# Optimization experiments

Hardware: AMD Instinct MI355X
Metric: run time of the kernel (lower is better)

## Reference

```python
import jax, jax.numpy as jnp
import numpy as np

D_MODEL = 512
N_HEADS = 8
D_K = D_MODEL // N_HEADS


def setup_inputs() -> dict:
    key = jax.random.key(0)
    ks = jax.random.split(key, 9)
    s = 1.0 / np.sqrt(D_MODEL)
    x = jax.random.normal(ks[0], (2, 4096, D_MODEL), dtype=jnp.float32)
    def lin(kw, kb):
        W = jax.random.uniform(kw, (D_MODEL, D_MODEL), jnp.float32, -s, s)
        b = jax.random.uniform(kb, (D_MODEL,), jnp.float32, -s, s)
        return W, b
    Wq, bq = lin(ks[1], ks[2])
    Wk, bk = lin(ks[3], ks[4])
    Wv, bv = lin(ks[5], ks[6])
    Wo, bo = lin(ks[7], ks[8])
    return {"x": x, "Wq": Wq, "bq": bq, "Wk": Wk, "bk": bk,
            "Wv": Wv, "bv": bv, "Wo": Wo, "bo": bo}


def reference(x, Wq, bq, Wk, bk, Wv, bv, Wo, bo):
    B, T, C = x.shape
    # project and split heads: [B, H, T, d_k]
    def heads(W, b):
        return (x @ W.T + b).reshape(B, T, N_HEADS, D_K).transpose(0, 2, 1, 3)
    q = heads(Wq, bq)
    k = heads(Wk, bk)
    v = heads(Wv, bv)
    scores = jnp.einsum('bhqd,bhkd->bhqk', q, k) / np.sqrt(D_K).astype(jnp.float32)
    attn = jax.nn.softmax(scores, axis=-1)  # dropout p=0 (eval)
    out = jnp.einsum('bhqk,bhkd->bhqd', attn, v)
    out = out.transpose(0, 2, 1, 3).reshape(B, T, C)
    return out @ Wo.T + bo
```

## Files before the change

kernel.cpp:

```cpp
#include <hip/hip_runtime.h>

typedef _Float16 f16x8 __attribute__((ext_vector_type(8)));
typedef _Float16 f16x4 __attribute__((ext_vector_type(4)));
typedef _Float16 f16x2 __attribute__((ext_vector_type(2)));
typedef __fp16 hf16x2 __attribute__((ext_vector_type(2)));
typedef float f32x4 __attribute__((ext_vector_type(4)));

__device__ __forceinline__ float fast_exp2(float x) {
#if __has_builtin(__builtin_amdgcn_exp2f)
  return __builtin_amdgcn_exp2f(x);
#else
  return exp2f(x);
#endif
}

__device__ __forceinline__ f16x2 pk_cvt(float a, float b) {
#if __has_builtin(__builtin_amdgcn_cvt_pkrtz)
  union { hf16x2 h; f16x2 f; } u;
  u.h = __builtin_amdgcn_cvt_pkrtz(a, b);
  return u.f;
#else
  f16x2 r; r[0] = (_Float16)a; r[1] = (_Float16)b; return r;
#endif
}

__device__ __forceinline__ void qswap32(int& x, int& y) {
  asm("v_permlane32_swap_b32 %0, %1" : "+v"(x), "+v"(y));
}

__device__ __forceinline__ int swz23(int c) {
  return (c & ~12) | ((c & 4) << 1) | ((c & 8) >> 1);
}

__global__ void cvt_all(const float* __restrict__ x,
                        const float* __restrict__ Wq, const float* __restrict__ Wk,
                        const float* __restrict__ Wv, const float* __restrict__ Wo,
                        _Float16* __restrict__ xf, _Float16* __restrict__ wf) {
  int g = blockIdx.x * blockDim.x + threadIdx.x;
  const float* src;
  _Float16* dst;
  if (g < 524288) {
    src = x + (size_t)g * 8;
    dst = xf + (size_t)g * 8;
  } else {
    int g2 = g - 524288;
    int z = g2 >> 15, off = g2 & 32767;
    const float* W = (z == 0) ? Wq : (z == 1) ? Wk : (z == 2) ? Wv : Wo;
    src = W + (size_t)off * 8;
    dst = wf + (size_t)z * 262144 + (size_t)off * 8;
  }
  f32x4 a = *(const f32x4*)src;
  f32x4 b = *(const f32x4*)(src + 4);
  f16x8 o;
  o[0] = (_Float16)a[0]; o[1] = (_Float16)a[1];
  o[2] = (_Float16)a[2]; o[3] = (_Float16)a[3];
  o[4] = (_Float16)b[0]; o[5] = (_Float16)b[1];
  o[6] = (_Float16)b[2]; o[7] = (_Float16)b[3];
  *(f16x8*)dst = o;
}

__global__ __launch_bounds__(256, 2)
void qkv_gemm(const _Float16* __restrict__ X, const _Float16* __restrict__ Wf,
              const float* __restrict__ bq, const float* __restrict__ bk,
              const float* __restrict__ bv, _Float16* __restrict__ dst3) {
  __shared__ __align__(16) _Float16 As[128][72];
  __shared__ __align__(16) _Float16 Bs[128][72];
  const int z = blockIdx.z;
  const _Float16* Wz = Wf + (size_t)z * 262144;
  const float* bias = (z == 0) ? bq : (z == 1 ? bk : bv);
  _Float16* dst = dst3 + (size_t)z * 4194304;
  const float scale = (z == 0) ? 0.18033688011112042f : 1.0f;

  const int t = threadIdx.x;
  const int lane = t & 63, wave = t >> 6;
  const int quad = lane >> 4, col = lane & 15;
  const int wm = (wave & 1) * 64, wn = (wave >> 1) * 64;
  const int m0 = blockIdx.x * 128, n0 = blockIdx.y * 128;

  f32x4 acc[4][4] = {};

  for (int k0 = 0; k0 < 512; k0 += 64) {
    __syncthreads();
#pragma unroll
    for (int i = 0; i < 4; i++) {
      int flat = i * 2048 + t * 8;
      int r = flat >> 6, c = flat & 63;
      *(f16x8*)&As[r][c] = *(const f16x8*)&X[(size_t)(m0 + r) * 512 + k0 + c];
      *(f16x8*)&Bs[r][c] = *(const f16x8*)&Wz[(size_t)(n0 + r) * 512 + k0 + c];
    }
    __syncthreads();
#pragma unroll
    for (int ks = 0; ks < 2; ks++) {
      f16x8 a[4], b[4];
#pragma unroll
      for (int i = 0; i < 4; i++) {
        a[i] = *(const f16x8*)&As[wm + i * 16 + col][ks * 32 + quad * 8];
        b[i] = *(const f16x8*)&Bs[wn + i * 16 + col][ks * 32 + quad * 8];
      }
      if (z != 2) {
#pragma unroll
        for (int mi = 0; mi < 4; mi++)
#pragma unroll
          for (int ni = 0; ni < 4; ni++)
            acc[mi][ni] = __builtin_amdgcn_mfma_f32_16x16x32_f16(b[ni], a[mi], acc[mi][ni], 0, 0, 0);
      } else {
#pragma unroll
        for (int mi = 0; mi < 4; mi++)
#pragma unroll
          for (int ni = 0; ni < 4; ni++)
            acc[mi][ni] = __builtin_amdgcn_mfma_f32_16x16x32_f16(a[mi], b[ni], acc[mi][ni], 0, 0, 0);
      }
    }
  }

  if (z != 2) {
#pragma unroll
    for (int ni = 0; ni < 4; ni++) {
      int nb = n0 + wn + ni * 16 + quad * 4;
      int h = nb >> 6, d0 = nb & 63;
      f32x4 bb = *(const f32x4*)&bias[nb];
#pragma unroll
      for (int mi = 0; mi < 4; mi++) {
        int m = m0 + wm + mi * 16 + col;
        int b = m >> 12, tt = m & 4095;
        f16x4 ov;
#pragma unroll
        for (int r = 0; r < 4; r++)
          ov[r] = (_Float16)((acc[mi][ni][r] + bb[r]) * scale);
        *(f16x4*)&dst[((size_t)(b * 8 + h) * 4096 + tt) * 64 + d0] = ov;
      }
    }
  } else {
#pragma unroll
    for (int ni = 0; ni < 4; ni++) {
      int n = n0 + wn + ni * 16 + col;
      float bv_ = bias[n];
      int h = n >> 6, d = n & 63;
#pragma unroll
      for (int mi = 0; mi < 4; mi++) {
        int m = m0 + wm + mi * 16 + quad * 4;
        int b = m >> 12, tt = m & 4095;
        f16x4 ov;
#pragma unroll
        for (int r = 0; r < 4; r++) ov[r] = (_Float16)(acc[mi][ni][r] + bv_);
        *(f16x4*)&dst[((size_t)((b * 8 + h) * 64 + d)) * 4096 + tt] = ov;
      }
    }
  }
}

__global__ __launch_bounds__(256, 2)
void attn_kernel(const _Float16* __restrict__ Q, const _Float16* __restrict__ K,
                 const _Float16* __restrict__ V, _Float16* __restrict__ O) {
  __shared__ __align__(16) _Float16 Ks[2][128][72];
  __shared__ __align__(16) _Float16 Vt[2][64][136];

  const int t = threadIdx.x;
  const int lane = t & 63, wave = t >> 6;
  const int quad = lane >> 4, col = lane & 15;
  const int id = blockIdx.y * 32 + blockIdx.x;
  const int xcd = id & 7, slot = id >> 3;
  const int bh = xcd * 2 + (slot >> 5);
  const int q0 = (slot & 31) * 128;
  const _Float16* Qb = Q + (size_t)bh * 4096 * 64;
  const _Float16* Kbh = K + (size_t)bh * 4096 * 64;
  const _Float16* Vg = V + (size_t)bh * 64 * 4096;

  const int sr = (t * 8) >> 6, sc = (t * 8) & 63;
  const int vrow = t >> 4, vcol = (t & 15) * 8;
  const int vc0 = swz23(vcol);
  const int vc1 = swz23(vcol + 4);

  f16x8 qf[2][2];
#pragma unroll
  for (int mt = 0; mt < 2; mt++)
#pragma unroll
    for (int ks = 0; ks < 2; ks++)
      qf[mt][ks] = *(const f16x8*)&Qb[(size_t)(q0 + wave * 32 + mt * 16 + col) * 64 +
                                      ks * 32 + quad * 8];

  const f32x4 fz = {0.f, 0.f, 0.f, 0.f};

  f16x8 kreg[4], vreg[4];
#pragma unroll
  for (int i = 0; i < 4; i++)
    kreg[i] = *(const f16x8*)&Kbh[(size_t)(sr + 32 * i) * 64 + sc];
#pragma unroll
  for (int it = 0; it < 4; it++)
    vreg[it] = *(const f16x8*)&Vg[(size_t)(it * 16 + vrow) * 4096 + vcol];
#pragma unroll
  for (int i = 0; i < 4; i++)
    *(f16x8*)&Ks[0][sr + 32 * i][sc] = kreg[i];
#pragma unroll
  for (int it = 0; it < 4; it++) {
    f16x4 lo, hi;
#pragma unroll
    for (int u = 0; u < 4; u++) { lo[u] = vreg[it][u]; hi[u] = vreg[it][u + 4]; }
    *(f16x4*)&Vt[0][it * 16 + vrow][vc0] = lo;
    *(f16x4*)&Vt[0][it * 16 + vrow][vc1] = hi;
  }
  __syncthreads();

  f32x4 o_acc[2][4] = {};
  float lsum[2] = {0.f, 0.f};

  for (int j = 0; j < 32; j++) {
    const int buf = j & 1;
    if (j + 1 < 32) {
      const _Float16* Kb = Kbh + (size_t)(j + 1) * 128 * 64;
#pragma unroll
      for (int i = 0; i < 4; i++)
        kreg[i] = *(const f16x8*)&Kb[(size_t)(sr + 32 * i) * 64 + sc];
#pragma unroll
      for (int it = 0; it < 4; it++)
        vreg[it] = *(const f16x8*)&Vg[(size_t)(it * 16 + vrow) * 4096 +
                                      (j + 1) * 128 + vcol];
    }

    f32x4 s[2][8];
    __builtin_amdgcn_s_setprio(1);
#pragma unroll
    for (int nt = 0; nt < 8; nt++) {
      f16x8 kf = *(const f16x8*)&Ks[buf][nt * 16 + col][quad * 8];
#pragma unroll
      for (int mt = 0; mt < 2; mt++)
        s[mt][nt] = __builtin_amdgcn_mfma_f32_16x16x32_f16(kf, qf[mt][0], fz, 0, 0, 0);
    }
#pragma unroll
    for (int nt = 0; nt < 8; nt++) {
      f16x8 kf = *(const f16x8*)&Ks[buf][nt * 16 + col][32 + quad * 8];
#pragma unroll
      for (int mt = 0; mt < 2; mt++)
        s[mt][nt] = __builtin_amdgcn_mfma_f32_16x16x32_f16(kf, qf[mt][1], s[mt][nt], 0, 0, 0);
    }
    __builtin_amdgcn_s_setprio(0);

    f16x4 pf[2][8];
#pragma unroll
    for (int mt = 0; mt < 2; mt++) {
#pragma unroll
      for (int nt = 0; nt < 8; nt++) {
        float p0 = fast_exp2(s[mt][nt][0]);
        float p1 = fast_exp2(s[mt][nt][1]);
        float p2 = fast_exp2(s[mt][nt][2]);
        float p3 = fast_exp2(s[mt][nt][3]);
        lsum[mt] += (p0 + p1) + (p2 + p3);
        union { f16x4 v4; f16x2 v2[2]; } u;
        u.v2[0] = pk_cvt(p0, p1);
        u.v2[1] = pk_cvt(p2, p3);
        pf[mt][nt] = u.v4;
      }
    }

    __builtin_amdgcn_s_setprio(1);
#pragma unroll
    for (int u = 0; u < 4; u++) {
      f16x8 p8[2];
#pragma unroll
      for (int mt = 0; mt < 2; mt++) {
        union { f16x4 v; int d[2]; } X, Y;
        X.v = pf[mt][2 * u]; Y.v = pf[mt][2 * u + 1];
        int x0 = X.d[0], y0 = Y.d[0], x1 = X.d[1], y1 = Y.d[1];
        qswap32(x0, y0);
        qswap32(x1, y1);
        union { int d[4]; f16x8 v; } P;
        P.d[0] = x0; P.d[1] = x1; P.d[2] = y0; P.d[3] = y1;
        p8[mt] = P.v;
      }
#pragma unroll
      for (int dt = 0; dt < 4; dt++) {
        f16x8 vf = *(const f16x8*)&Vt[buf][dt * 16 + col][u * 32 + quad * 8];
#pragma unroll
        for (int mt = 0; mt < 2; mt++)
          o_acc[mt][dt] = __builtin_amdgcn_mfma_f32_16x16x32_f16(vf, p8[mt], o_acc[mt][dt], 0, 0, 0);
      }
    }
    __builtin_amdgcn_s_setprio(0);

    if (j + 1 < 32) {
      const int nb = buf ^ 1;
#pragma unroll
      for (int i = 0; i < 4; i++)
        *(f16x8*)&Ks[nb][sr + 32 * i][sc] = kreg[i];
#pragma unroll
      for (int it = 0; it < 4; it++) {
        f16x4 lo, hi;
#pragma unroll
        for (int u = 0; u < 4; u++) { lo[u] = vreg[it][u]; hi[u] = vreg[it][u + 4]; }
        *(f16x4*)&Vt[nb][it * 16 + vrow][vc0] = lo;
        *(f16x4*)&Vt[nb][it * 16 + vrow][vc1] = hi;
      }
      __syncthreads();
    }
  }

  const int b = bh >> 3, h = bh & 7;
#pragma unroll
  for (int mt = 0; mt < 2; mt++) {
    float l = lsum[mt];
    l += __shfl_xor(l, 16, 64);
    l += __shfl_xor(l, 32, 64);
    int row = q0 + wave * 32 + mt * 16 + col;
    float inv = 1.0f / l;
#pragma unroll
    for (int dt = 0; dt < 4; dt++) {
      f16x4 ov;
#pragma unroll
      for (int r = 0; r < 4; r++) ov[r] = (_Float16)(o_acc[mt][dt][r] * inv);
      *(f16x4*)&O[((size_t)(b * 4096 + row)) * 512 + h * 64 + dt * 16 + quad * 4] = ov;
    }
  }
}

__global__ __launch_bounds__(256, 2)
void out_gemm(const _Float16* __restrict__ X, const _Float16* __restrict__ Wo,
              const float* __restrict__ bias, float* __restrict__ out) {
  __shared__ __align__(16) _Float16 As[128][72];
  __shared__ __align__(16) _Float16 Bs[128][72];
  const int t = threadIdx.x;
  const int lane = t & 63, wave = t >> 6;
  const int quad = lane >> 4, col = lane & 15;
  const int wm = (wave & 1) * 64, wn = (wave >> 1) * 64;
  const int m0 = blockIdx.x * 128, n0 = blockIdx.y * 128;

  f32x4 acc[4][4] = {};

  for (int k0 = 0; k0 < 512; k0 += 64) {
    __syncthreads();
#pragma unroll
    for (int i = 0; i < 4; i++) {
      int flat = i * 2048 + t * 8;
      int r = flat >> 6, c = flat & 63;
      *(f16x8*)&As[r][c] = *(const f16x8*)&X[(size_t)(m0 + r) * 512 + k0 + c];
      *(f16x8*)&Bs[r][c] = *(const f16x8*)&Wo[(size_t)(n0 + r) * 512 + k0 + c];
    }
    __syncthreads();
#pragma unroll
    for (int ks = 0; ks < 2; ks++) {
      f16x8 a[4], b[4];
#pragma unroll
      for (int i = 0; i < 4; i++) {
        a[i] = *(const f16x8*)&As[wm + i * 16 + col][ks * 32 + quad * 8];
        b[i] = *(const f16x8*)&Bs[wn + i * 16 + col][ks * 32 + quad * 8];
      }
#pragma unroll
      for (int mi = 0; mi < 4; mi++)
#pragma unroll
        for (int ni = 0; ni < 4; ni++)
          acc[mi][ni] = __builtin_amdgcn_mfma_f32_16x16x32_f16(a[mi], b[ni], acc[mi][ni], 0, 0, 0);
    }
  }

#pragma unroll
  for (int ni = 0; ni < 4; ni++) {
    int n = n0 + wn + ni * 16 + col;
    float bv_ = bias[n];
#pragma unroll
    for (int mi = 0; mi < 4; mi++) {
#pragma unroll
      for (int r = 0; r < 4; r++) {
        int m = m0 + wm + mi * 16 + quad * 4 + r;
        out[(size_t)m * 512 + n] = acc[mi][ni][r] + bv_;
      }
    }
  }
}

extern "C" void kernel_launch(void* const* d_in, const int* in_sizes, int n_in,
                              void* d_out, int out_size, void* d_ws, size_t ws_size,
                              hipStream_t stream) {
  const float* x  = (const float*)d_in[0];
  const float* Wq = (const float*)d_in[1];
  const float* bq = (const float*)d_in[2];
  const float* Wk = (const float*)d_in[3];
  const float* bk = (const float*)d_in[4];
  const float* Wv = (const float*)d_in[5];
  const float* bv = (const float*)d_in[6];
  const float* Wo = (const float*)d_in[7];
  const float* bo = (const float*)d_in[8];

  char* ws = (char*)d_ws;
  _Float16* xf  = (_Float16*)(ws);
  _Float16* wf  = (_Float16*)(ws + (8u << 20));
  _Float16* qkv = (_Float16*)(ws + (10u << 20));
  _Float16* ao  = (_Float16*)(ws);

  cvt_all<<<2560, 256, 0, stream>>>(x, Wq, Wk, Wv, Wo, xf, wf);

  qkv_gemm<<<dim3(64, 4, 3), 256, 0, stream>>>(xf, wf, bq, bk, bv, qkv);

  attn_kernel<<<dim3(32, 16), 256, 0, stream>>>(qkv, qkv + 4194304,
                                                qkv + 2 * 4194304, ao);

  out_gemm<<<dim3(64, 4), 256, 0, stream>>>(ao, wf + 3 * 262144, bo,
                                            (float*)d_out);
}
```

Baseline: 205.6 us.

## Double-buffer GEMM tiles, remap blocks per XCD, vectorize out_gemm stores

Both projection GEMMs now keep two LDS tile buffers and prefetch the next K slice into registers while the current slice runs on MFMA, so each step needs one barrier instead of two. Block indices are remapped so consecutive M tiles land on the same XCD, which should improve L2 reuse. out_gemm swaps its MFMA operand order so each lane holds contiguous columns, allowing 16-byte float4 stores with a vector bias load instead of scalar strided stores. The extra buffer doubles LDS per block and the prefetch registers raise register pressure.

```diff
diff --git a/kernel.cpp b/kernel.cpp
--- a/kernel.cpp
+++ b/kernel.cpp
@@ -63,9 +63,14 @@
 void qkv_gemm(const _Float16* __restrict__ X, const _Float16* __restrict__ Wf,
               const float* __restrict__ bq, const float* __restrict__ bk,
               const float* __restrict__ bv, _Float16* __restrict__ dst3) {
-  __shared__ __align__(16) _Float16 As[128][72];
-  __shared__ __align__(16) _Float16 Bs[128][72];
-  const int z = blockIdx.z;
+  __shared__ __align__(16) _Float16 As[2][128][72];
+  __shared__ __align__(16) _Float16 Bs[2][128][72];
+  const int id = (blockIdx.z * 4 + blockIdx.y) * 64 + blockIdx.x;
+  const int xcd = id & 7, s = id >> 3;
+  const int m0 = (xcd * 8 + (s & 7)) * 128;
+  const int yz = s >> 3;
+  const int n0 = (yz & 3) * 128;
+  const int z = yz >> 2;
   const _Float16* Wz = Wf + (size_t)z * 262144;
   const float* bias = (z == 0) ? bq : (z == 1 ? bk : bv);
   _Float16* dst = dst3 + (size_t)z * 4194304;
@@ -75,45 +80,68 @@
   const int lane = t & 63, wave = t >> 6;
   const int quad = lane >> 4, col = lane & 15;
   const int wm = (wave & 1) * 64, wn = (wave >> 1) * 64;
-  const int m0 = blockIdx.x * 128, n0 = blockIdx.y * 128;
+  const int sr = (t * 8) >> 6, sc = (t * 8) & 63;
 
   f32x4 acc[4][4] = {};
-
-  for (int k0 = 0; k0 < 512; k0 += 64) {
+  f16x8 areg[4], breg[4];
+
+#define GLOAD(K0)                                                             \
+  {                                                                           \
+    _Pragma("unroll") for (int i = 0; i < 4; i++) {                           \
+      areg[i] = *(const f16x8*)&X[(size_t)(m0 + sr + 32 * i) * 512 + (K0) + sc]; \
+      breg[i] = *(const f16x8*)&Wz[(size_t)(n0 + sr + 32 * i) * 512 + (K0) + sc]; \
+    }                                                                         \
+  }
+
+#define GSTAGE(B)                                                             \
+  {                                                                           \
+    _Pragma("unroll") for (int i = 0; i < 4; i++) {                           \
+      *(f16x8*)&As[(B)][sr + 32 * i][sc] = areg[i];                           \
+      *(f16x8*)&Bs[(B)][sr + 32 * i][sc] = breg[i];                           \
+    }                                                                         \
+  }
+
+#define GCOMP_QK(B)                                                           \
+  {                                                                           \
+    _Pragma("unroll") for (int ks = 0; ks < 2; ks++) {                        \
+      f16x8 a[4], b[4];                                                       \
+      _Pragma("unroll") for (int i = 0; i < 4; i++) {                         \
+        a[i] = *(const f16x8*)&As[(B)][wm + i * 16 + col][ks * 32 + quad * 8]; \
+        b[i] = *(const f16x8*)&Bs[(B)][wn + i * 16 + col][ks * 32 + quad * 8]; \
+      }                                                                       \
+      _Pragma("unroll") for (int mi = 0; mi < 4; mi++)                        \
+        _Pragma("unroll") for (int ni = 0; ni < 4; ni++)                      \
+          acc[mi][ni] = __builtin_amdgcn_mfma_f32_16x16x32_f16(               \
+              b[ni], a[mi], acc[mi][ni], 0, 0, 0);                            \
+    }                                                                         \
+  }
+
+#define GCOMP_V(B)                                                            \
+  {                                                                           \
+    _Pragma("unroll") for (int ks = 0; ks < 2; ks++) {                        \
+      f16x8 a[4], b[4];                                                       \
+      _Pragma("unroll") for (int i = 0; i < 4; i++) {                         \
+        a[i] = *(const f16x8*)&As[(B)][wm + i * 16 + col][ks * 32 + quad * 8]; \
+        b[i] = *(const f16x8*)&Bs[(B)][wn + i * 16 + col][ks * 32 + quad * 8]; \
+      }                                                                       \
+      _Pragma("unroll") for (int mi = 0; mi < 4; mi++)                        \
+        _Pragma("unroll") for (int ni = 0; ni < 4; ni++)                      \
+          acc[mi][ni] = __builtin_amdgcn_mfma_f32_16x16x32_f16(               \
+              a[mi], b[ni], acc[mi][ni], 0, 0, 0);                            \
+    }                                                                         \
+  }
+
+  if (z != 2) {
+    GLOAD(0); GSTAGE(0); GLOAD(64);
     __syncthreads();
-#pragma unroll
-    for (int i = 0; i < 4; i++) {
-      int flat = i * 2048 + t * 8;
-      int r = flat >> 6, c = flat & 63;
-      *(f16x8*)&As[r][c] = *(const f16x8*)&X[(size_t)(m0 + r) * 512 + k0 + c];
-      *(f16x8*)&Bs[r][c] = *(const f16x8*)&Wz[(size_t)(n0 + r) * 512 + k0 + c];
-    }
-    __syncthreads();
-#pragma unroll
-    for (int ks = 0; ks < 2; ks++) {
-      f16x8 a[4], b[4];
-#pragma unroll
-      for (int i = 0; i < 4; i++) {
-        a[i] = *(const f16x8*)&As[wm + i * 16 + col][ks * 32 + quad * 8];
-        b[i] = *(const f16x8*)&Bs[wn + i * 16 + col][ks * 32 + quad * 8];
-      }
-      if (z != 2) {
-#pragma unroll
-        for (int mi = 0; mi < 4; mi++)
-#pragma unroll
-          for (int ni = 0; ni < 4; ni++)
-            acc[mi][ni] = __builtin_amdgcn_mfma_f32_16x16x32_f16(b[ni], a[mi], acc[mi][ni], 0, 0, 0);
-      } else {
-#pragma unroll
-        for (int mi = 0; mi < 4; mi++)
-#pragma unroll
-          for (int ni = 0; ni < 4; ni++)
-            acc[mi][ni] = __builtin_amdgcn_mfma_f32_16x16x32_f16(a[mi], b[ni], acc[mi][ni], 0, 0, 0);
-      }
-    }
-  }
-
-  if (z != 2) {
+    GCOMP_QK(0);
+    GSTAGE(1); GLOAD(128); __syncthreads(); GCOMP_QK(1);
+    GSTAGE(0); GLOAD(192); __syncthreads(); GCOMP_QK(0);
+    GSTAGE(1); GLOAD(256); __syncthreads(); GCOMP_QK(1);
+    GSTAGE(0); GLOAD(320); __syncthreads(); GCOMP_QK(0);
+    GSTAGE(1); GLOAD(384); __syncthreads(); GCOMP_QK(1);
+    GSTAGE(0); GLOAD(448); __syncthreads(); GCOMP_QK(0);
+    GSTAGE(1); __syncthreads(); GCOMP_QK(1);
 #pragma unroll
     for (int ni = 0; ni < 4; ni++) {
       int nb = n0 + wn + ni * 16 + quad * 4;
@@ -131,6 +159,16 @@
       }
     }
   } else {
+    GLOAD(0); GSTAGE(0); GLOAD(64);
+    __syncthreads();
+    GCOMP_V(0);
+    GSTAGE(1); GLOAD(128); __syncthreads(); GCOMP_V(1);
+    GSTAGE(0); GLOAD(192); __syncthreads(); GCOMP_V(0);
+    GSTAGE(1); GLOAD(256); __syncthreads(); GCOMP_V(1);
+    GSTAGE(0); GLOAD(320); __syncthreads(); GCOMP_V(0);
+    GSTAGE(1); GLOAD(384); __syncthreads(); GCOMP_V(1);
+    GSTAGE(0); GLOAD(448); __syncthreads(); GCOMP_V(0);
+    GSTAGE(1); __syncthreads(); GCOMP_V(1);
 #pragma unroll
     for (int ni = 0; ni < 4; ni++) {
       int n = n0 + wn + ni * 16 + col;
@@ -147,6 +185,10 @@
       }
     }
   }
+#undef GLOAD
+#undef GSTAGE
+#undef GCOMP_QK
+#undef GCOMP_V
 }
 
 __global__ __launch_bounds__(256, 2)
@@ -315,53 +357,78 @@
 __global__ __launch_bounds__(256, 2)
 void out_gemm(const _Float16* __restrict__ X, const _Float16* __restrict__ Wo,
               const float* __restrict__ bias, float* __restrict__ out) {
-  __shared__ __align__(16) _Float16 As[128][72];
-  __shared__ __align__(16) _Float16 Bs[128][72];
+  __shared__ __align__(16) _Float16 As[2][128][72];
+  __shared__ __align__(16) _Float16 Bs[2][128][72];
+  const int id = blockIdx.y * 64 + blockIdx.x;
+  const int xcd = id & 7, s = id >> 3;
+  const int m0 = (xcd * 8 + (s & 7)) * 128;
+  const int n0 = (s >> 3) * 128;
+
   const int t = threadIdx.x;
   const int lane = t & 63, wave = t >> 6;
   const int quad = lane >> 4, col = lane & 15;
   const int wm = (wave & 1) * 64, wn = (wave >> 1) * 64;
-  const int m0 = blockIdx.x * 128, n0 = blockIdx.y * 128;
+  const int sr = (t * 8) >> 6, sc = (t * 8) & 63;
 
   f32x4 acc[4][4] = {};
-
-  for (int k0 = 0; k0 < 512; k0 += 64) {
-    __syncthreads();
-#pragma unroll
-    for (int i = 0; i < 4; i++) {
-      int flat = i * 2048 + t * 8;
-      int r = flat >> 6, c = flat & 63;
-      *(f16x8*)&As[r][c] = *(const f16x8*)&X[(size_t)(m0 + r) * 512 + k0 + c];
-      *(f16x8*)&Bs[r][c] = *(const f16x8*)&Wo[(size_t)(n0 + r) * 512 + k0 + c];
-    }
-    __syncthreads();
-#pragma unroll
-    for (int ks = 0; ks < 2; ks++) {
-      f16x8 a[4], b[4];
-#pragma unroll
-      for (int i = 0; i < 4; i++) {
-        a[i] = *(const f16x8*)&As[wm + i * 16 + col][ks * 32 + quad * 8];
-        b[i] = *(const f16x8*)&Bs[wn + i * 16 + col][ks * 32 + quad * 8];
-      }
-#pragma unroll
-      for (int mi = 0; mi < 4; mi++)
-#pragma unroll
-        for (int ni = 0; ni < 4; ni++)
-          acc[mi][ni] = __builtin_amdgcn_mfma_f32_16x16x32_f16(a[mi], b[ni], acc[mi][ni], 0, 0, 0);
-    }
-  }
+  f16x8 areg[4], breg[4];
+
+#define OLOAD(K0)                                                             \
+  {                                                                           \
+    _Pragma("unroll") for (int i = 0; i < 4; i++) {                           \
+      areg[i] = *(const f16x8*)&X[(size_t)(m0 + sr + 32 * i) * 512 + (K0) + sc]; \
+      breg[i] = *(const f16x8*)&Wo[(size_t)(n0 + sr + 32 * i) * 512 + (K0) + sc]; \
+    }                                                                         \
+  }
+
+#define OSTAGE(B)                                                             \
+  {                                                                           \
+    _Pragma("unroll") for (int i = 0; i < 4; i++) {                           \
+      *(f16x8*)&As[(B)][sr + 32 * i][sc] = areg[i];                           \
+      *(f16x8*)&Bs[(B)][sr + 32 * i][sc] = breg[i];                           \
+    }                                                                         \
+  }
+
+#define OCOMP(B)                                                              \
+  {                                                                           \
+    _Pragma("unroll") for (int ks = 0; ks < 2; ks++) {                        \
+      f16x8 a[4], b[4];                                                       \
+      _Pragma("unroll") for (int i = 0; i < 4; i++) {                         \
+        a[i] = *(const f16x8*)&As[(B)][wm + i * 16 + col][ks * 32 + quad * 8]; \
+        b[i] = *(const f16x8*)&Bs[(B)][wn + i * 16 + col][ks * 32 + quad * 8]; \
+      }                                                                       \
+      _Pragma("unroll") for (int mi = 0; mi < 4; mi++)                        \
+        _Pragma("unroll") for (int ni = 0; ni < 4; ni++)                      \
+          acc[mi][ni] = __builtin_amdgcn_mfma_f32_16x16x32_f16(               \
+              b[ni], a[mi], acc[mi][ni], 0, 0, 0);                            \
+    }                                                                         \
+  }
+
+  OLOAD(0); OSTAGE(0); OLOAD(64);
+  __syncthreads();
+  OCOMP(0);
+  OSTAGE(1); OLOAD(128); __syncthreads(); OCOMP(1);
+  OSTAGE(0); OLOAD(192); __syncthreads(); OCOMP(0);
+  OSTAGE(1); OLOAD(256); __syncthreads(); OCOMP(1);
+  OSTAGE(0); OLOAD(320); __syncthreads(); OCOMP(0);
+  OSTAGE(1); OLOAD(384); __syncthreads(); OCOMP(1);
+  OSTAGE(0); OLOAD(448); __syncthreads(); OCOMP(0);
+  OSTAGE(1); __syncthreads(); OCOMP(1);
+#undef OLOAD
+#undef OSTAGE
+#undef OCOMP
 
 #pragma unroll
   for (int ni = 0; ni < 4; ni++) {
-    int n = n0 + wn + ni * 16 + col;
-    float bv_ = bias[n];
+    int nb = n0 + wn + ni * 16 + quad * 4;
+    f32x4 bb = *(const f32x4*)&bias[nb];
 #pragma unroll
     for (int mi = 0; mi < 4; mi++) {
-#pragma unroll
-      for (int r = 0; r < 4; r++) {
-        int m = m0 + wm + mi * 16 + quad * 4 + r;
-        out[(size_t)m * 512 + n] = acc[mi][ni][r] + bv_;
-      }
+      int m = m0 + wm + mi * 16 + col;
+      f32x4 ov;
+#pragma unroll
+      for (int r = 0; r < 4; r++) ov[r] = acc[mi][ni][r] + bb[r];
+      *(f32x4*)&out[(size_t)m * 512 + nb] = ov;
     }
   }
 }
@@ -392,6 +459,6 @@
   attn_kernel<<<dim3(32, 16), 256, 0, stream>>>(qkv, qkv + 4194304,
                                                 qkv + 2 * 4194304, ao);
 
-  out_gemm<<<dim3(64, 4), 256, 0, stream>>>(ao, wf + 3 * 262144, bo,
+  out_gemm<<<dim3(64, 4), 256, 0, stream>>>(ao, Wo == nullptr ? nullptr : wf + 3 * 262144, bo,
                                             (float*)d_out);
 }
```

Result: faster. 192.2 us (-6.5%).
